# Kernel tuning notes

Measured on AMD Instinct MI355X. Metric: run time of the kernel, lower is better.

Reference implementation:

```python
import jax, jax.numpy as jnp
import numpy as np

B, T, I, H, L = 32768, 30, 4, 64, 32


def _lstm_layer(x, Wih, Whh, bih, bhh):
    """PyTorch-semantics single-layer LSTM, batch_first. Returns (outputs [B,T,H], h_T [B,H])."""
    # Precompute input contribution for all timesteps: [B, T, 4H]
    xg = jnp.einsum('bti,gi->btg', x, Wih) + bih + bhh
    Hh = Whh.shape[1]
    h0 = jnp.zeros((x.shape[0], Hh), x.dtype)

    def step(carry, xg_t):
        h, c = carry
        g = xg_t + h @ Whh.T  # [B, 4H]
        i, f, gg, o = jnp.split(g, 4, axis=-1)  # PyTorch gate order i,f,g,o
        c = jax.nn.sigmoid(f) * c + jax.nn.sigmoid(i) * jnp.tanh(gg)
        h = jax.nn.sigmoid(o) * jnp.tanh(c)
        return (h, c), h

    (hT, _), hs = jax.lax.scan(step, (h0, h0), jnp.swapaxes(xg, 0, 1))
    return jnp.swapaxes(hs, 0, 1), hT


def setup_inputs() -> dict:
    key = jax.random.key(0)
    ks = jax.random.split(key, 20)
    s = 0.1  # weight scale for numerical stability
    inp = {
        'x': jax.random.normal(ks[0], (B, T, I), jnp.float32),
        'enc1_Wih': s * jax.random.normal(ks[1], (4 * H, I), jnp.float32),
        'enc1_Whh': s * jax.random.normal(ks[2], (4 * H, H), jnp.float32),
        'enc1_bih': s * jax.random.normal(ks[3], (4 * H,), jnp.float32),
        'enc1_bhh': s * jax.random.normal(ks[4], (4 * H,), jnp.float32),
        'enc2_Wih': s * jax.random.normal(ks[5], (4 * L, H), jnp.float32),
        'enc2_Whh': s * jax.random.normal(ks[6], (4 * L, L), jnp.float32),
        'enc2_bih': s * jax.random.normal(ks[7], (4 * L,), jnp.float32),
        'enc2_bhh': s * jax.random.normal(ks[8], (4 * L,), jnp.float32),
        'dec1_Wih': s * jax.random.normal(ks[9], (4 * H, L), jnp.float32),
        'dec1_Whh': s * jax.random.normal(ks[10], (4 * H, H), jnp.float32),
        'dec1_bih': s * jax.random.normal(ks[11], (4 * H,), jnp.float32),
        'dec1_bhh': s * jax.random.normal(ks[12], (4 * H,), jnp.float32),
        'dec2_Wih': s * jax.random.normal(ks[13], (4 * I, H), jnp.float32),
        'dec2_Whh': s * jax.random.normal(ks[14], (4 * I, I), jnp.float32),
        'dec2_bih': s * jax.random.normal(ks[15], (4 * I,), jnp.float32),
        'dec2_bhh': s * jax.random.normal(ks[16], (4 * I,), jnp.float32),
    }
    return inp


def reference(x, enc1_Wih, enc1_Whh, enc1_bih, enc1_bhh,
              enc2_Wih, enc2_Whh, enc2_bih, enc2_bhh,
              dec1_Wih, dec1_Whh, dec1_bih, dec1_bhh,
              dec2_Wih, dec2_Whh, dec2_bih, dec2_bhh):
    seq_len = x.shape[1]
    out, _ = _lstm_layer(x, enc1_Wih, enc1_Whh, enc1_bih, enc1_bhh)
    out, h = _lstm_layer(out, enc2_Wih, enc2_Whh, enc2_bih, enc2_bhh)
    latent = jnp.repeat(h[:, None, :], seq_len, axis=1)  # [B, T, L]
    out, _ = _lstm_layer(latent, dec1_Wih, dec1_Whh, dec1_bih, dec1_bhh)
    out, _ = _lstm_layer(out, dec2_Wih, dec2_Whh, dec2_bih, dec2_bhh)
    return out
```

## Files before the change

kernel.cpp:

```cpp
#include <hip/hip_runtime.h>
#include <stdint.h>


typedef unsigned short u16;
typedef unsigned int u32;
typedef __attribute__((ext_vector_type(8))) short bf16x8;
typedef __attribute__((ext_vector_type(4))) float f32x4;
typedef __attribute__((ext_vector_type(4))) u32 u32x4;
typedef __attribute__((ext_vector_type(2))) u32 u32x2;

#define BATCH 32768
#define TT 30
#define IN 4
#define WAVES 8
#define BLOCKT (WAVES * 64)
#define MB 16
#define BPB (WAVES * MB)

#define LOG2E 1.4426950408889634f
#define LOG2E2 2.8853900817779268f

#define O_WHH1 0
#define O_W1C  8192
#define O_WIH2 9216
#define O_WHH2 13312
#define O_WHH3 0
#define O_WIH3 8192
#define O_WIH4 12288
#define O_W4HHF 12800
#define O_B1F 15360
#define O_B2F 15616
#define O_B3F 15744
#define O_B4F 16000
#define O_BUFS 16016
#define PBUF 1600
#define SMEM_WORDS (O_BUFS + WAVES * PBUF)
#define SMEM_BYTES (SMEM_WORDS * 4)

#define WB() __builtin_amdgcn_wave_barrier()
#define MFMA(a, b, c) __builtin_amdgcn_mfma_f32_16x16x32_bf16((a), (b), (c), 0, 0, 0)

__device__ __forceinline__ u16 f2bf(float f) {
    u32 u = __float_as_uint(f);
    u += 0x7fffu + ((u >> 16) & 1u);
    return (u16)(u >> 16);
}
__device__ __forceinline__ float bf2f(u16 v) { return __uint_as_float(((u32)v) << 16); }

__device__ __forceinline__ u32 cvtpk2(float a, float b) {
    u32 d;
    asm("v_cvt_pk_bf16_f32 %0, %1, %2" : "=v"(d) : "v"(a), "v"(b));
    return d;
}

__device__ __forceinline__ float unitH(float yi, float yf, float yg, float yo, float& c) {
    const float ei = __builtin_amdgcn_exp2f(-yi);
    const float ef = __builtin_amdgcn_exp2f(-yf);
    const float eg = __builtin_amdgcn_exp2f(yg);
    const float eo = __builtin_amdgcn_exp2f(-yo);
    const float Z = (1.f + ei) * (1.f + eg);
    const float X = 1.f + ef;
    const float num = fmaf(eg - 1.f, X, c * Z);
    c = num * __builtin_amdgcn_rcpf(X * Z);
    const float ec = __builtin_amdgcn_exp2f(c * LOG2E2);
    return (ec - 1.f) * __builtin_amdgcn_rcpf((1.f + eo) * (1.f + ec));
}

template <int KT, int GS>
__device__ __forceinline__ void stageBh(u16* hi, const float* src, int N, int tid) {
    const int K = KT * 32;
    const int total = N * K;
    for (int idx = tid; idx < total; idx += BLOCKT) {
        const int j = idx & 7;
        const int l = (idx >> 3) & 63;
        const int pr = idx >> 9;
        const int kt = pr & (KT - 1);
        const int nt = pr / KT;
        const int n = (nt << 4) | (l & 15);
        const int k = (kt << 5) + ((l >> 4) << 3) + j;
        const float s = (((n >> GS) & 3) == 2) ? LOG2E2 : LOG2E;
        hi[idx] = f2bf(src[n * K + k] * s);
    }
}

__global__ __launch_bounds__(BLOCKT)
__attribute__((amdgpu_waves_per_eu(2)))
void lstm_ae(
    const float* __restrict__ x,
    const float* __restrict__ w1ih, const float* __restrict__ w1hh,
    const float* __restrict__ b1i, const float* __restrict__ b1h,
    const float* __restrict__ w2ih, const float* __restrict__ w2hh,
    const float* __restrict__ b2i, const float* __restrict__ b2h,
    const float* __restrict__ w3ih, const float* __restrict__ w3hh,
    const float* __restrict__ b3i, const float* __restrict__ b3h,
    const float* __restrict__ w4ih, const float* __restrict__ w4hh,
    const float* __restrict__ b4i, const float* __restrict__ b4h,
    float* __restrict__ out) {
    extern __shared__ float smem[];
    float* W = smem;

    const int tid = threadIdx.x;
    const int wave = tid >> 6, lane = tid & 63;
    const int col = lane & 15, quad = lane >> 4;

    float* pb = smem + O_BUFS + wave * PBUF;
    u16* h1d = (u16*)pb;
    u16* h2b = (u16*)(pb + 1024);
    float* gbuf = pb + 1280;
    float* bufH4 = pb + 1536;

    const int b0w = blockIdx.x * BPB + wave * MB;
    const int hbase = (col << 3) + ((quad & 1) << 2) + ((quad >> 1) << 7);

    stageBh<2, 6>((u16*)(W + O_WHH1), w1hh, 256, tid);
    stageBh<2, 5>((u16*)(W + O_WIH2), w2ih, 128, tid);
    stageBh<1, 5>((u16*)(W + O_WHH2), w2hh, 128, tid);
    {
        u16* C = (u16*)(W + O_W1C);
        for (int idx = tid; idx < 2048; idx += BLOCKT) {
            const int n = idx >> 3, j = idx & 7;
            const float sc = ((n >> 6) == 2) ? LOG2E2 : LOG2E;
            const float w = w1ih[n * 4 + (j & 3)] * sc;
            C[idx] = (j < 4) ? f2bf(w) : f2bf(w - bf2f(f2bf(w)));
        }
    }
    float* b1f = W + O_B1F;
    float* b2f = W + O_B2F;
    float* b3f = W + O_B3F;
    float* b4f = W + O_B4F;
    for (int i = tid; i < 256; i += BLOCKT)
        b1f[i] = (b1i[i] + b1h[i]) * (((i >> 6) == 2) ? LOG2E2 : LOG2E);
    for (int i = tid; i < 128; i += BLOCKT)
        b2f[i] = (b2i[i] + b2h[i]) * (((i >> 5) == 2) ? LOG2E2 : LOG2E);
    for (int i = tid; i < 256; i += BLOCKT)
        b3f[i] = (b3i[i] + b3h[i]) * (((i >> 6) == 2) ? LOG2E2 : LOG2E);
    for (int i = tid; i < 16; i += BLOCKT)
        b4f[i] = (b4i[i] + b4h[i]) * (((i >> 2) == 2) ? LOG2E2 : LOG2E);
    {
        u32* z = (u32*)pb;
        for (int i = lane; i < 256; i += 64) z[1024 + i] = 0u;
        bufH4[lane] = 0.f;
    }
    __syncthreads();

    const u16* Whh1hi = (const u16*)(W + O_WHH1);
    const u16* Wih2hi = (const u16*)(W + O_WIH2);
    const u16* Whh2hi = (const u16*)(W + O_WHH2);
    const u16* W1cL = (const u16*)(W + O_W1C) + (col << 3) + ((quad == 1) ? 4 : 0);

    f32x4 b2r[8];
#pragma unroll
    for (int nt = 0; nt < 8; ++nt)
        b2r[nt] = *reinterpret_cast<const f32x4*>(b2f + nt * 16 + (quad << 2));

    float c1[4][4];
    float c2[2][4];
#pragma unroll
    for (int q = 0; q < 4; ++q)
#pragma unroll
        for (int r = 0; r < 4; ++r) c1[q][r] = 0.f;
#pragma unroll
    for (int q = 0; q < 2; ++q)
#pragma unroll
        for (int r = 0; r < 4; ++r) c2[q][r] = 0.f;

    float4 xcur = *reinterpret_cast<const float4*>(x + ((size_t)(b0w + col) * TT + 0) * IN);

    auto enc1_step = [&](const bf16x8 ah0, const bf16x8 ah1, u16* hnext, int tnext) {
        const float4 xc = xcur;
        {
            const int tn = (tnext + 1 < TT) ? tnext + 1 : tnext;
            xcur = *reinterpret_cast<const float4*>(x + ((size_t)(b0w + col) * TT + tn) * IN);
        }
        const u32 hi01 = cvtpk2(xc.x, xc.y);
        const u32 hi23 = cvtpk2(xc.z, xc.w);
        const float r0 = xc.x - __uint_as_float(hi01 << 16);
        const float r1 = xc.y - __uint_as_float(hi01 & 0xffff0000u);
        const float r2 = xc.z - __uint_as_float(hi23 << 16);
        const float r3 = xc.w - __uint_as_float(hi23 & 0xffff0000u);
        const u32 lo01 = cvtpk2(r0, r1);
        const u32 lo23 = cvtpk2(r2, r3);
        u32x4 xv;
        xv.x = (quad <= 1) ? hi01 : 0u;
        xv.y = (quad <= 1) ? hi23 : 0u;
        xv.z = (quad == 0) ? lo01 : 0u;
        xv.w = (quad == 0) ? lo23 : 0u;
        const bf16x8 a1x = __builtin_bit_cast(bf16x8, xv);
#pragma unroll
        for (int q = 0; q < 4; ++q) {
            f32x4 acc[4];
#pragma unroll
            for (int i = 0; i < 4; ++i) {
                const int nt = i * 4 + q;
                const u32x2 wp = *reinterpret_cast<const u32x2*>(W1cL + nt * 128);
                u32x4 afu;
                afu.x = wp.x; afu.y = wp.y; afu.z = wp.x; afu.w = wp.y;
                const bf16x8 af = __builtin_bit_cast(bf16x8, afu);
                const bf16x8 bh0 = *reinterpret_cast<const bf16x8*>(Whh1hi + ((nt * 2 + 0) * 64 + lane) * 8);
                const bf16x8 bh1 = *reinterpret_cast<const bf16x8*>(Whh1hi + ((nt * 2 + 1) * 64 + lane) * 8);
                f32x4 a = *reinterpret_cast<const f32x4*>(b1f + nt * 16 + (quad << 2));
                a = MFMA(af, a1x, a);
                a = MFMA(bh0, ah0, a);
                a = MFMA(bh1, ah1, a);
                acc[i] = a;
            }
            const float h0 = unitH(acc[0][0], acc[1][0], acc[2][0], acc[3][0], c1[q][0]);
            const float h1 = unitH(acc[0][1], acc[1][1], acc[2][1], acc[3][1], c1[q][1]);
            const float h2 = unitH(acc[0][2], acc[1][2], acc[2][2], acc[3][2], c1[q][2]);
            const float h3 = unitH(acc[0][3], acc[1][3], acc[2][3], acc[3][3], c1[q][3]);
            u32x2 wv;
            wv.x = cvtpk2(h0, h1);
            wv.y = cvtpk2(h2, h3);
            *reinterpret_cast<u32x2*>(hnext + hbase + ((q >> 1) << 9) + ((q & 1) << 8)) = wv;
        }
    };

    {
        const bf16x8 z8 = {};
        enc1_step(z8, z8, h1d, 0);
    }
    for (int t = 0; t < TT - 1; ++t) {
        const u16* hcur = h1d + ((t & 1) << 10);
        const bf16x8 ah0 = *reinterpret_cast<const bf16x8*>(hcur + lane * 8);
        const bf16x8 ah1 = *reinterpret_cast<const bf16x8*>(hcur + (64 + lane) * 8);
        const bf16x8 a2h = *reinterpret_cast<const bf16x8*>(h2b + lane * 8);
        f32x4 acc2[8];
#pragma unroll
        for (int nt = 0; nt < 8; ++nt) {
            const bf16x8 bh0 = *reinterpret_cast<const bf16x8*>(Wih2hi + ((nt * 2 + 0) * 64 + lane) * 8);
            const bf16x8 bh1 = *reinterpret_cast<const bf16x8*>(Wih2hi + ((nt * 2 + 1) * 64 + lane) * 8);
            const bf16x8 ch = *reinterpret_cast<const bf16x8*>(Whh2hi + (nt * 64 + lane) * 8);
            f32x4 a = b2r[nt];
            a = MFMA(bh0, ah0, a);
            a = MFMA(bh1, ah1, a);
            a = MFMA(ch, a2h, a);
            acc2[nt] = a;
        }
        enc1_step(ah0, ah1, h1d + (((t + 1) & 1) << 10), t + 1);
#pragma unroll
        for (int q = 0; q < 2; ++q) {
            const float h0 = unitH(acc2[q][0], acc2[2 + q][0], acc2[4 + q][0], acc2[6 + q][0], c2[q][0]);
            const float h1 = unitH(acc2[q][1], acc2[2 + q][1], acc2[4 + q][1], acc2[6 + q][1], c2[q][1]);
            const float h2 = unitH(acc2[q][2], acc2[2 + q][2], acc2[4 + q][2], acc2[6 + q][2], c2[q][2]);
            const float h3 = unitH(acc2[q][3], acc2[2 + q][3], acc2[4 + q][3], acc2[6 + q][3], c2[q][3]);
            u32x2 wv;
            wv.x = cvtpk2(h0, h1);
            wv.y = cvtpk2(h2, h3);
            *reinterpret_cast<u32x2*>(h2b + hbase + (q << 8)) = wv;
        }
    }
    {
        const u16* hcur = h1d + (((TT - 1) & 1) << 10);
        const bf16x8 ah0 = *reinterpret_cast<const bf16x8*>(hcur + lane * 8);
        const bf16x8 ah1 = *reinterpret_cast<const bf16x8*>(hcur + (64 + lane) * 8);
        const bf16x8 a2h = *reinterpret_cast<const bf16x8*>(h2b + lane * 8);
        f32x4 acc2[8];
#pragma unroll
        for (int nt = 0; nt < 8; ++nt) {
            const bf16x8 bh0 = *reinterpret_cast<const bf16x8*>(Wih2hi + ((nt * 2 + 0) * 64 + lane) * 8);
            const bf16x8 bh1 = *reinterpret_cast<const bf16x8*>(Wih2hi + ((nt * 2 + 1) * 64 + lane) * 8);
            const bf16x8 ch = *reinterpret_cast<const bf16x8*>(Whh2hi + (nt * 64 + lane) * 8);
            f32x4 a = b2r[nt];
            a = MFMA(bh0, ah0, a);
            a = MFMA(bh1, ah1, a);
            a = MFMA(ch, a2h, a);
            acc2[nt] = a;
        }
#pragma unroll
        for (int q = 0; q < 2; ++q) {
            const float h0 = unitH(acc2[q][0], acc2[2 + q][0], acc2[4 + q][0], acc2[6 + q][0], c2[q][0]);
            const float h1 = unitH(acc2[q][1], acc2[2 + q][1], acc2[4 + q][1], acc2[6 + q][1], c2[q][1]);
            const float h2 = unitH(acc2[q][2], acc2[2 + q][2], acc2[4 + q][2], acc2[6 + q][2], c2[q][2]);
            const float h3 = unitH(acc2[q][3], acc2[2 + q][3], acc2[4 + q][3], acc2[6 + q][3], c2[q][3]);
            u32x2 wv;
            wv.x = cvtpk2(h0, h1);
            wv.y = cvtpk2(h2, h3);
            *reinterpret_cast<u32x2*>(h2b + hbase + (q << 8)) = wv;
        }
    }

    __syncthreads();
    stageBh<2, 6>((u16*)(W + O_WHH3), w3hh, 256, tid);
    stageBh<1, 6>((u16*)(W + O_WIH3), w3ih, 256, tid);
    stageBh<2, 2>((u16*)(W + O_WIH4), w4ih, 16, tid);
    for (int i = tid; i < 64; i += BLOCKT)
        W[O_W4HHF + i] = w4hh[i] * ((((i >> 4) & 3) == 2) ? LOG2E2 : LOG2E);

    const bf16x8 aLh = *reinterpret_cast<const bf16x8*>(h2b + lane * 8);
    float c3[4][4];
#pragma unroll
    for (int q = 0; q < 4; ++q)
#pragma unroll
        for (int r = 0; r < 4; ++r) c3[q][r] = 0.f;
    float c4 = 0.f;
    const int u4 = lane & 3, mb = lane >> 2;
    __syncthreads();

    const u16* Whh3hi = (const u16*)(W + O_WHH3);
    const u16* Wih3hi = (const u16*)(W + O_WIH3);
    f32x4 b3r[16];
#pragma unroll
    for (int nt = 0; nt < 16; ++nt)
        b3r[nt] = *reinterpret_cast<const f32x4*>(b3f + nt * 16 + (quad << 2));
    const f32x4 bias4v = *reinterpret_cast<const f32x4*>(b4f + (quad << 2));
    const bf16x8 w4f0 = *reinterpret_cast<const bf16x8*>((const u16*)(W + O_WIH4) + (0 * 64 + lane) * 8);
    const bf16x8 w4f1 = *reinterpret_cast<const bf16x8*>((const u16*)(W + O_WIH4) + (1 * 64 + lane) * 8);
    float4 w4r[4];
#pragma unroll
    for (int r = 0; r < 4; ++r)
        w4r[r] = *reinterpret_cast<const float4*>(W + O_W4HHF + ((quad * 4 + r) << 2));

    auto dec1_step = [&](const bf16x8 ah0, const bf16x8 ah1, u16* hnext) {
#pragma unroll
        for (int q = 0; q < 4; ++q) {
            f32x4 acc[4];
#pragma unroll
            for (int i = 0; i < 4; ++i) {
                const int nt = i * 4 + q;
                const bf16x8 bL = *reinterpret_cast<const bf16x8*>(Wih3hi + (nt * 64 + lane) * 8);
                const bf16x8 bh0 = *reinterpret_cast<const bf16x8*>(Whh3hi + ((nt * 2 + 0) * 64 + lane) * 8);
                const bf16x8 bh1 = *reinterpret_cast<const bf16x8*>(Whh3hi + ((nt * 2 + 1) * 64 + lane) * 8);
                f32x4 a = MFMA(bL, aLh, b3r[nt]);
                a = MFMA(bh0, ah0, a);
                a = MFMA(bh1, ah1, a);
                acc[i] = a;
            }
            const float h0 = unitH(acc[0][0], acc[1][0], acc[2][0], acc[3][0], c3[q][0]);
            const float h1 = unitH(acc[0][1], acc[1][1], acc[2][1], acc[3][1], c3[q][1]);
            const float h2 = unitH(acc[0][2], acc[1][2], acc[2][2], acc[3][2], c3[q][2]);
            const float h3 = unitH(acc[0][3], acc[1][3], acc[2][3], acc[3][3], c3[q][3]);
            u32x2 wv;
            wv.x = cvtpk2(h0, h1);
            wv.y = cvtpk2(h2, h3);
            *reinterpret_cast<u32x2*>(hnext + hbase + ((q >> 1) << 9) + ((q & 1) << 8)) = wv;
        }
    };

    {
        const bf16x8 z8 = {};
        dec1_step(z8, z8, h1d);
    }
    for (int t = 0; t < TT - 1; ++t) {
        const u16* hcur = h1d + ((t & 1) << 10);
        const bf16x8 ah0 = *reinterpret_cast<const bf16x8*>(hcur + lane * 8);
        const bf16x8 ah1 = *reinterpret_cast<const bf16x8*>(hcur + (64 + lane) * 8);
        f32x4 acc4 = bias4v;
        {
            const float4 hv = *reinterpret_cast<const float4*>(bufH4 + (col << 2));
#pragma unroll
            for (int r = 0; r < 4; ++r) {
                float sa = acc4[r];
                sa = fmaf(w4r[r].x, hv.x, sa);
                sa = fmaf(w4r[r].y, hv.y, sa);
                sa = fmaf(w4r[r].z, hv.z, sa);
                sa = fmaf(w4r[r].w, hv.w, sa);
                acc4[r] = sa;
            }
        }
        acc4 = MFMA(w4f0, ah0, acc4);
        acc4 = MFMA(w4f1, ah1, acc4);
        dec1_step(ah0, ah1, h1d + (((t + 1) & 1) << 10));
        WB();
        *reinterpret_cast<f32x4*>(gbuf + (col << 4) + (quad << 2)) = acc4;
        WB();
        {
            const float yi = gbuf[mb * 16 + u4];
            const float yf = gbuf[mb * 16 + 4 + u4];
            const float yg = gbuf[mb * 16 + 8 + u4];
            const float yo = gbuf[mb * 16 + 12 + u4];
            const float h = unitH(yi, yf, yg, yo, c4);
            out[((size_t)(b0w + mb) * TT + t) * IN + u4] = h;
            bufH4[mb * 4 + u4] = h;
        }
    }
    {
        const int t = TT - 1;
        const u16* hcur = h1d + ((t & 1) << 10);
        const bf16x8 ah0 = *reinterpret_cast<const bf16x8*>(hcur + lane * 8);
        const bf16x8 ah1 = *reinterpret_cast<const bf16x8*>(hcur + (64 + lane) * 8);
        f32x4 acc4 = bias4v;
        {
            const float4 hv = *reinterpret_cast<const float4*>(bufH4 + (col << 2));
#pragma unroll
            for (int r = 0; r < 4; ++r) {
                float sa = acc4[r];
                sa = fmaf(w4r[r].x, hv.x, sa);
                sa = fmaf(w4r[r].y, hv.y, sa);
                sa = fmaf(w4r[r].z, hv.z, sa);
                sa = fmaf(w4r[r].w, hv.w, sa);
                acc4[r] = sa;
            }
        }
        acc4 = MFMA(w4f0, ah0, acc4);
        acc4 = MFMA(w4f1, ah1, acc4);
        WB();
        *reinterpret_cast<f32x4*>(gbuf + (col << 4) + (quad << 2)) = acc4;
        WB();
        {
            const float yi = gbuf[mb * 16 + u4];
            const float yf = gbuf[mb * 16 + 4 + u4];
            const float yg = gbuf[mb * 16 + 8 + u4];
            const float yo = gbuf[mb * 16 + 12 + u4];
            const float h = unitH(yi, yf, yg, yo, c4);
            out[((size_t)(b0w + mb) * TT + t) * IN + u4] = h;
        }
    }
}

extern "C" void kernel_launch(void* const* d_in, const int* in_sizes, int n_in,
                              void* d_out, int out_size, void* d_ws, size_t ws_size,
                              hipStream_t stream) {
    (void)in_sizes; (void)n_in; (void)d_ws; (void)ws_size; (void)out_size;
    hipFuncSetAttribute(reinterpret_cast<const void*>(lstm_ae),
                        hipFuncAttributeMaxDynamicSharedMemorySize, SMEM_BYTES);
    const float* xi = (const float*)d_in[0];
    const float* w1ih = (const float*)d_in[1];
    const float* w1hh = (const float*)d_in[2];
    const float* b1i = (const float*)d_in[3];
    const float* b1h = (const float*)d_in[4];
    const float* w2ih = (const float*)d_in[5];
    const float* w2hh = (const float*)d_in[6];
    const float* b2i = (const float*)d_in[7];
    const float* b2h = (const float*)d_in[8];
    const float* w3ih = (const float*)d_in[9];
    const float* w3hh = (const float*)d_in[10];
    const float* b3i = (const float*)d_in[11];
    const float* b3h = (const float*)d_in[12];
    const float* w4ih = (const float*)d_in[13];
    const float* w4hh = (const float*)d_in[14];
    const float* b4i = (const float*)d_in[15];
    const float* b4h = (const float*)d_in[16];
    float* out = (float*)d_out;

    lstm_ae<<<dim3(BATCH / BPB), dim3(BLOCKT), SMEM_BYTES, stream>>>(
        xi, w1ih, w1hh, b1i, b1h, w2ih, w2hh, b2i, b2h,
        w3ih, w3hh, b3i, b3h, w4ih, w4hh, b4i, b4h, out);
}
```

Measured before the change: 299.2 us.

## Interleave LSTM gate MFMAs with activation tails and fold enc1 bias into MFMA

```diff
diff --git a/kernel.cpp b/kernel.cpp
--- a/kernel.cpp
+++ b/kernel.cpp
@@ -22,17 +22,16 @@
 
 #define O_WHH1 0
 #define O_W1C  8192
-#define O_WIH2 9216
-#define O_WHH2 13312
+#define O_WIH2 10240
+#define O_WHH2 14336
 #define O_WHH3 0
 #define O_WIH3 8192
 #define O_WIH4 12288
 #define O_W4HHF 12800
-#define O_B1F 15360
-#define O_B2F 15616
-#define O_B3F 15744
-#define O_B4F 16000
-#define O_BUFS 16016
+#define O_B2F 16384
+#define O_B3F 16512
+#define O_B4F 16768
+#define O_BUFS 16784
 #define PBUF 1600
 #define SMEM_WORDS (O_BUFS + WAVES * PBUF)
 #define SMEM_BYTES (SMEM_WORDS * 4)
@@ -82,6 +81,74 @@
         hi[idx] = f2bf(src[n * K + k] * s);
     }
 }
+
+#define ENC1_MFMA(Q, ACC, A1X, AH0, AH1)                                                   \
+    _Pragma("unroll") for (int i_ = 0; i_ < 4; ++i_) {                                     \
+        const int nt_ = i_ * 4 + (Q);                                                      \
+        const bf16x8 bh0_ = *reinterpret_cast<const bf16x8*>(Whh1hi + ((nt_ * 2 + 0) * 64 + lane) * 8); \
+        const bf16x8 bh1_ = *reinterpret_cast<const bf16x8*>(Whh1hi + ((nt_ * 2 + 1) * 64 + lane) * 8); \
+        f32x4 a_ = MFMA(w1a[nt_], (A1X), zf);                                              \
+        a_ = MFMA(bh0_, (AH0), a_);                                                        \
+        a_ = MFMA(bh1_, (AH1), a_);                                                        \
+        (ACC)[i_] = a_;                                                                    \
+    }
+
+#define ENC1_TAIL(Q, ACC, HOUT) {                                                          \
+        const float h0_ = unitH((ACC)[0][0], (ACC)[1][0], (ACC)[2][0], (ACC)[3][0], c1[Q][0]); \
+        const float h1_ = unitH((ACC)[0][1], (ACC)[1][1], (ACC)[2][1], (ACC)[3][1], c1[Q][1]); \
+        const float h2_ = unitH((ACC)[0][2], (ACC)[1][2], (ACC)[2][2], (ACC)[3][2], c1[Q][2]); \
+        const float h3_ = unitH((ACC)[0][3], (ACC)[1][3], (ACC)[2][3], (ACC)[3][3], c1[Q][3]); \
+        u32x2 wv_;                                                                         \
+        wv_.x = cvtpk2(h0_, h1_);                                                          \
+        wv_.y = cvtpk2(h2_, h3_);                                                          \
+        *reinterpret_cast<u32x2*>((HOUT) + hbase + (((Q) >> 1) << 9) + (((Q) & 1) << 8)) = wv_; \
+    }
+
+#define ENC2_BURST(AH0, AH1, A2H, ACC2)                                                    \
+    _Pragma("unroll") for (int nt_ = 0; nt_ < 8; ++nt_) {                                  \
+        const bf16x8 bh0_ = *reinterpret_cast<const bf16x8*>(Wih2hi + ((nt_ * 2 + 0) * 64 + lane) * 8); \
+        const bf16x8 bh1_ = *reinterpret_cast<const bf16x8*>(Wih2hi + ((nt_ * 2 + 1) * 64 + lane) * 8); \
+        const bf16x8 ch_ = *reinterpret_cast<const bf16x8*>(Whh2hi + (nt_ * 64 + lane) * 8); \
+        f32x4 a_ = b2r[nt_];                                                               \
+        a_ = MFMA(bh0_, (AH0), a_);                                                        \
+        a_ = MFMA(bh1_, (AH1), a_);                                                        \
+        a_ = MFMA(ch_, (A2H), a_);                                                         \
+        (ACC2)[nt_] = a_;                                                                  \
+    }
+
+#define ENC2_TAIL(ACC2)                                                                    \
+    _Pragma("unroll") for (int q_ = 0; q_ < 2; ++q_) {                                     \
+        const float h0_ = unitH((ACC2)[q_][0], (ACC2)[2 + q_][0], (ACC2)[4 + q_][0], (ACC2)[6 + q_][0], c2[q_][0]); \
+        const float h1_ = unitH((ACC2)[q_][1], (ACC2)[2 + q_][1], (ACC2)[4 + q_][1], (ACC2)[6 + q_][1], c2[q_][1]); \
+        const float h2_ = unitH((ACC2)[q_][2], (ACC2)[2 + q_][2], (ACC2)[4 + q_][2], (ACC2)[6 + q_][2], c2[q_][2]); \
+        const float h3_ = unitH((ACC2)[q_][3], (ACC2)[2 + q_][3], (ACC2)[4 + q_][3], (ACC2)[6 + q_][3], c2[q_][3]); \
+        u32x2 wv_;                                                                         \
+        wv_.x = cvtpk2(h0_, h1_);                                                          \
+        wv_.y = cvtpk2(h2_, h3_);                                                          \
+        *reinterpret_cast<u32x2*>(h2b + hbase + (q_ << 8)) = wv_;                          \
+    }
+
+#define DEC1_MFMA(Q, ACC, AH0, AH1)                                                        \
+    _Pragma("unroll") for (int i_ = 0; i_ < 4; ++i_) {                                     \
+        const int nt_ = i_ * 4 + (Q);                                                      \
+        const bf16x8 bh0_ = *reinterpret_cast<const bf16x8*>(Whh3hi + ((nt_ * 2 + 0) * 64 + lane) * 8); \
+        const bf16x8 bh1_ = *reinterpret_cast<const bf16x8*>(Whh3hi + ((nt_ * 2 + 1) * 64 + lane) * 8); \
+        f32x4 a_ = MFMA(wih3r[nt_], aLh, b3r[nt_]);                                        \
+        a_ = MFMA(bh0_, (AH0), a_);                                                        \
+        a_ = MFMA(bh1_, (AH1), a_);                                                        \
+        (ACC)[i_] = a_;                                                                    \
+    }
+
+#define DEC1_TAIL(Q, ACC, HOUT) {                                                          \
+        const float h0_ = unitH((ACC)[0][0], (ACC)[1][0], (ACC)[2][0], (ACC)[3][0], c3[Q][0]); \
+        const float h1_ = unitH((ACC)[0][1], (ACC)[1][1], (ACC)[2][1], (ACC)[3][1], c3[Q][1]); \
+        const float h2_ = unitH((ACC)[0][2], (ACC)[1][2], (ACC)[2][2], (ACC)[3][2], c3[Q][2]); \
+        const float h3_ = unitH((ACC)[0][3], (ACC)[1][3], (ACC)[2][3], (ACC)[3][3], c3[Q][3]); \
+        u32x2 wv_;                                                                         \
+        wv_.x = cvtpk2(h0_, h1_);                                                          \
+        wv_.y = cvtpk2(h2_, h3_);                                                          \
+        *reinterpret_cast<u32x2*>((HOUT) + hbase + (((Q) >> 1) << 9) + (((Q) & 1) << 8)) = wv_; \
+    }
 
 __global__ __launch_bounds__(BLOCKT)
 __attribute__((amdgpu_waves_per_eu(2)))
@@ -117,19 +184,27 @@
     stageBh<1, 5>((u16*)(W + O_WHH2), w2hh, 128, tid);
     {
         u16* C = (u16*)(W + O_W1C);
-        for (int idx = tid; idx < 2048; idx += BLOCKT) {
-            const int n = idx >> 3, j = idx & 7;
+        for (int idx = tid; idx < 256 * 16; idx += BLOCKT) {
+            const int n = idx >> 4, j = idx & 15;
             const float sc = ((n >> 6) == 2) ? LOG2E2 : LOG2E;
-            const float w = w1ih[n * 4 + (j & 3)] * sc;
-            C[idx] = (j < 4) ? f2bf(w) : f2bf(w - bf2f(f2bf(w)));
-        }
-    }
-    float* b1f = W + O_B1F;
+            u16 v = 0;
+            if (j < 4) {
+                v = f2bf(w1ih[n * 4 + j] * sc);
+            } else if (j < 8) {
+                const float w = w1ih[n * 4 + (j - 4)] * sc;
+                v = f2bf(w - bf2f(f2bf(w)));
+            } else if (j == 8) {
+                v = f2bf((b1i[n] + b1h[n]) * sc);
+            } else if (j == 9) {
+                const float b = (b1i[n] + b1h[n]) * sc;
+                v = f2bf(b - bf2f(f2bf(b)));
+            }
+            C[idx] = v;
+        }
+    }
     float* b2f = W + O_B2F;
     float* b3f = W + O_B3F;
     float* b4f = W + O_B4F;
-    for (int i = tid; i < 256; i += BLOCKT)
-        b1f[i] = (b1i[i] + b1h[i]) * (((i >> 6) == 2) ? LOG2E2 : LOG2E);
     for (int i = tid; i < 128; i += BLOCKT)
         b2f[i] = (b2i[i] + b2h[i]) * (((i >> 5) == 2) ? LOG2E2 : LOG2E);
     for (int i = tid; i < 256; i += BLOCKT)
@@ -146,8 +221,26 @@
     const u16* Whh1hi = (const u16*)(W + O_WHH1);
     const u16* Wih2hi = (const u16*)(W + O_WIH2);
     const u16* Whh2hi = (const u16*)(W + O_WHH2);
-    const u16* W1cL = (const u16*)(W + O_W1C) + (col << 3) + ((quad == 1) ? 4 : 0);
-
+
+    bf16x8 w1a[16];
+    {
+        const u16* Cx = (const u16*)(W + O_W1C);
+#pragma unroll
+        for (int nt = 0; nt < 16; ++nt) {
+            const u16* row = Cx + (((nt << 4) | col) << 4);
+            u32x4 v = {0u, 0u, 0u, 0u};
+            if (quad == 0) {
+                const u32x2 p = *reinterpret_cast<const u32x2*>(row);
+                v.x = p.x; v.y = p.y; v.z = p.x; v.w = p.y;
+            } else if (quad == 1) {
+                const u32x2 p = *reinterpret_cast<const u32x2*>(row + 4);
+                v.x = p.x; v.y = p.y; v.z = p.x; v.w = p.y;
+            } else if (quad == 2) {
+                v.x = *reinterpret_cast<const u32*>(row + 8);
+            }
+            w1a[nt] = __builtin_bit_cast(bf16x8, v);
+        }
+    }
     f32x4 b2r[8];
 #pragma unroll
     for (int nt = 0; nt < 8; ++nt)
@@ -164,14 +257,10 @@
 #pragma unroll
         for (int r = 0; r < 4; ++r) c2[q][r] = 0.f;
 
+    const f32x4 zf = {0.f, 0.f, 0.f, 0.f};
     float4 xcur = *reinterpret_cast<const float4*>(x + ((size_t)(b0w + col) * TT + 0) * IN);
 
-    auto enc1_step = [&](const bf16x8 ah0, const bf16x8 ah1, u16* hnext, int tnext) {
-        const float4 xc = xcur;
-        {
-            const int tn = (tnext + 1 < TT) ? tnext + 1 : tnext;
-            xcur = *reinterpret_cast<const float4*>(x + ((size_t)(b0w + col) * TT + tn) * IN);
-        }
+    auto buildX = [&](const float4 xc) -> bf16x8 {
         const u32 hi01 = cvtpk2(xc.x, xc.y);
         const u32 hi23 = cvtpk2(xc.z, xc.w);
         const float r0 = xc.x - __uint_as_float(hi01 << 16);
@@ -181,73 +270,51 @@
         const u32 lo01 = cvtpk2(r0, r1);
         const u32 lo23 = cvtpk2(r2, r3);
         u32x4 xv;
-        xv.x = (quad <= 1) ? hi01 : 0u;
+        xv.x = (quad <= 1) ? hi01 : ((quad == 2) ? 0x3F803F80u : 0u);
         xv.y = (quad <= 1) ? hi23 : 0u;
         xv.z = (quad == 0) ? lo01 : 0u;
         xv.w = (quad == 0) ? lo23 : 0u;
-        const bf16x8 a1x = __builtin_bit_cast(bf16x8, xv);
-#pragma unroll
-        for (int q = 0; q < 4; ++q) {
-            f32x4 acc[4];
-#pragma unroll
-            for (int i = 0; i < 4; ++i) {
-                const int nt = i * 4 + q;
-                const u32x2 wp = *reinterpret_cast<const u32x2*>(W1cL + nt * 128);
-                u32x4 afu;
-                afu.x = wp.x; afu.y = wp.y; afu.z = wp.x; afu.w = wp.y;
-                const bf16x8 af = __builtin_bit_cast(bf16x8, afu);
-                const bf16x8 bh0 = *reinterpret_cast<const bf16x8*>(Whh1hi + ((nt * 2 + 0) * 64 + lane) * 8);
-                const bf16x8 bh1 = *reinterpret_cast<const bf16x8*>(Whh1hi + ((nt * 2 + 1) * 64 + lane) * 8);
-                f32x4 a = *reinterpret_cast<const f32x4*>(b1f + nt * 16 + (quad << 2));
-                a = MFMA(af, a1x, a);
-                a = MFMA(bh0, ah0, a);
-                a = MFMA(bh1, ah1, a);
-                acc[i] = a;
-            }
-            const float h0 = unitH(acc[0][0], acc[1][0], acc[2][0], acc[3][0], c1[q][0]);
-            const float h1 = unitH(acc[0][1], acc[1][1], acc[2][1], acc[3][1], c1[q][1]);
-            const float h2 = unitH(acc[0][2], acc[1][2], acc[2][2], acc[3][2], c1[q][2]);
-            const float h3 = unitH(acc[0][3], acc[1][3], acc[2][3], acc[3][3], c1[q][3]);
-            u32x2 wv;
-            wv.x = cvtpk2(h0, h1);
-            wv.y = cvtpk2(h2, h3);
-            *reinterpret_cast<u32x2*>(hnext + hbase + ((q >> 1) << 9) + ((q & 1) << 8)) = wv;
-        }
+        return __builtin_bit_cast(bf16x8, xv);
     };
 
     {
         const bf16x8 z8 = {};
-        enc1_step(z8, z8, h1d, 0);
+        const bf16x8 a1x = buildX(xcur);
+        xcur = *reinterpret_cast<const float4*>(x + ((size_t)(b0w + col) * TT + 1) * IN);
+        f32x4 accA[4], accB[4];
+        ENC1_MFMA(0, accA, a1x, z8, z8)
+        ENC1_MFMA(1, accB, a1x, z8, z8)
+        ENC1_TAIL(0, accA, h1d)
+        ENC1_MFMA(2, accA, a1x, z8, z8)
+        ENC1_TAIL(1, accB, h1d)
+        ENC1_MFMA(3, accB, a1x, z8, z8)
+        ENC1_TAIL(2, accA, h1d)
+        ENC1_TAIL(3, accB, h1d)
     }
     for (int t = 0; t < TT - 1; ++t) {
         const u16* hcur = h1d + ((t & 1) << 10);
+        u16* hnext = h1d + (((t + 1) & 1) << 10);
         const bf16x8 ah0 = *reinterpret_cast<const bf16x8*>(hcur + lane * 8);
         const bf16x8 ah1 = *reinterpret_cast<const bf16x8*>(hcur + (64 + lane) * 8);
         const bf16x8 a2h = *reinterpret_cast<const bf16x8*>(h2b + lane * 8);
         f32x4 acc2[8];
-#pragma unroll
-        for (int nt = 0; nt < 8; ++nt) {
-            const bf16x8 bh0 = *reinterpret_cast<const bf16x8*>(Wih2hi + ((nt * 2 + 0) * 64 + lane) * 8);
-            const bf16x8 bh1 = *reinterpret_cast<const bf16x8*>(Wih2hi + ((nt * 2 + 1) * 64 + lane) * 8);
-            const bf16x8 ch = *reinterpret_cast<const bf16x8*>(Whh2hi + (nt * 64 + lane) * 8);
-            f32x4 a = b2r[nt];
-            a = MFMA(bh0, ah0, a);
-            a = MFMA(bh1, ah1, a);
-            a = MFMA(ch, a2h, a);
-            acc2[nt] = a;
-        }
-        enc1_step(ah0, ah1, h1d + (((t + 1) & 1) << 10), t + 1);
-#pragma unroll
-        for (int q = 0; q < 2; ++q) {
-            const float h0 = unitH(acc2[q][0], acc2[2 + q][0], acc2[4 + q][0], acc2[6 + q][0], c2[q][0]);
-            const float h1 = unitH(acc2[q][1], acc2[2 + q][1], acc2[4 + q][1], acc2[6 + q][1], c2[q][1]);
-            const float h2 = unitH(acc2[q][2], acc2[2 + q][2], acc2[4 + q][2], acc2[6 + q][2], c2[q][2]);
-            const float h3 = unitH(acc2[q][3], acc2[2 + q][3], acc2[4 + q][3], acc2[6 + q][3], c2[q][3]);
-            u32x2 wv;
-            wv.x = cvtpk2(h0, h1);
-            wv.y = cvtpk2(h2, h3);
-            *reinterpret_cast<u32x2*>(h2b + hbase + (q << 8)) = wv;
-        }
+        ENC2_BURST(ah0, ah1, a2h, acc2)
+        const bf16x8 a1x = buildX(xcur);
+        {
+            const int tn = (t + 2 < TT) ? t + 2 : TT - 1;
+            xcur = *reinterpret_cast<const float4*>(x + ((size_t)(b0w + col) * TT + tn) * IN);
+        }
+        f32x4 accA[4], accB[4];
+        ENC1_MFMA(0, accA, a1x, ah0, ah1)
+        WB();
+        ENC2_TAIL(acc2)
+        ENC1_MFMA(1, accB, a1x, ah0, ah1)
+        ENC1_TAIL(0, accA, hnext)
+        ENC1_MFMA(2, accA, a1x, ah0, ah1)
+        ENC1_TAIL(1, accB, hnext)
+        ENC1_MFMA(3, accB, a1x, ah0, ah1)
+        ENC1_TAIL(2, accA, hnext)
+        ENC1_TAIL(3, accB, hnext)
     }
     {
         const u16* hcur = h1d + (((TT - 1) & 1) << 10);
@@ -255,28 +322,9 @@
         const bf16x8 ah1 = *reinterpret_cast<const bf16x8*>(hcur + (64 + lane) * 8);
         const bf16x8 a2h = *reinterpret_cast<const bf16x8*>(h2b + lane * 8);
         f32x4 acc2[8];
-#pragma unroll
-        for (int nt = 0; nt < 8; ++nt) {
-            const bf16x8 bh0 = *reinterpret_cast<const bf16x8*>(Wih2hi + ((nt * 2 + 0) * 64 + lane) * 8);
-            const bf16x8 bh1 = *reinterpret_cast<const bf16x8*>(Wih2hi + ((nt * 2 + 1) * 64 + lane) * 8);
-            const bf16x8 ch = *reinterpret_cast<const bf16x8*>(Whh2hi + (nt * 64 + lane) * 8);
-            f32x4 a = b2r[nt];
-            a = MFMA(bh0, ah0, a);
-            a = MFMA(bh1, ah1, a);
-            a = MFMA(ch, a2h, a);
-            acc2[nt] = a;
-        }
-#pragma unroll
-        for (int q = 0; q < 2; ++q) {
-            const float h0 = unitH(acc2[q][0], acc2[2 + q][0], acc2[4 + q][0], acc2[6 + q][0], c2[q][0]);
-            const float h1 = unitH(acc2[q][1], acc2[2 + q][1], acc2[4 + q][1], acc2[6 + q][1], c2[q][1]);
-            const float h2 = unitH(acc2[q][2], acc2[2 + q][2], acc2[4 + q][2], acc2[6 + q][2], c2[q][2]);
-            const float h3 = unitH(acc2[q][3], acc2[2 + q][3], acc2[4 + q][3], acc2[6 + q][3], c2[q][3]);
-            u32x2 wv;
-            wv.x = cvtpk2(h0, h1);
-            wv.y = cvtpk2(h2, h3);
-            *reinterpret_cast<u32x2*>(h2b + hbase + (q << 8)) = wv;
-        }
+        ENC2_BURST(ah0, ah1, a2h, acc2)
+        WB();
+        ENC2_TAIL(acc2)
     }
 
     __syncthreads();
@@ -298,6 +346,10 @@
 
     const u16* Whh3hi = (const u16*)(W + O_WHH3);
     const u16* Wih3hi = (const u16*)(W + O_WIH3);
+    bf16x8 wih3r[16];
+#pragma unroll
+    for (int nt = 0; nt < 16; ++nt)
+        wih3r[nt] = *reinterpret_cast<const bf16x8*>(Wih3hi + (nt * 64 + lane) * 8);
     f32x4 b3r[16];
 #pragma unroll
     for (int nt = 0; nt < 16; ++nt)
@@ -310,38 +362,21 @@
     for (int r = 0; r < 4; ++r)
         w4r[r] = *reinterpret_cast<const float4*>(W + O_W4HHF + ((quad * 4 + r) << 2));
 
-    auto dec1_step = [&](const bf16x8 ah0, const bf16x8 ah1, u16* hnext) {
-#pragma unroll
-        for (int q = 0; q < 4; ++q) {
-            f32x4 acc[4];
-#pragma unroll
-            for (int i = 0; i < 4; ++i) {
-                const int nt = i * 4 + q;
-                const bf16x8 bL = *reinterpret_cast<const bf16x8*>(Wih3hi + (nt * 64 + lane) * 8);
-                const bf16x8 bh0 = *reinterpret_cast<const bf16x8*>(Whh3hi + ((nt * 2 + 0) * 64 + lane) * 8);
-                const bf16x8 bh1 = *reinterpret_cast<const bf16x8*>(Whh3hi + ((nt * 2 + 1) * 64 + lane) * 8);
-                f32x4 a = MFMA(bL, aLh, b3r[nt]);
-                a = MFMA(bh0, ah0, a);
-                a = MFMA(bh1, ah1, a);
-                acc[i] = a;
-            }
-            const float h0 = unitH(acc[0][0], acc[1][0], acc[2][0], acc[3][0], c3[q][0]);
-            const float h1 = unitH(acc[0][1], acc[1][1], acc[2][1], acc[3][1], c3[q][1]);
-            const float h2 = unitH(acc[0][2], acc[1][2], acc[2][2], acc[3][2], c3[q][2]);
-            const float h3 = unitH(acc[0][3], acc[1][3], acc[2][3], acc[3][3], c3[q][3]);
-            u32x2 wv;
-            wv.x = cvtpk2(h0, h1);
-            wv.y = cvtpk2(h2, h3);
-            *reinterpret_cast<u32x2*>(hnext + hbase + ((q >> 1) << 9) + ((q & 1) << 8)) = wv;
-        }
-    };
-
     {
         const bf16x8 z8 = {};
-        dec1_step(z8, z8, h1d);
+        f32x4 accA[4], accB[4];
+        DEC1_MFMA(0, accA, z8, z8)
+        DEC1_MFMA(1, accB, z8, z8)
+        DEC1_TAIL(0, accA, h1d)
+        DEC1_MFMA(2, accA, z8, z8)
+        DEC1_TAIL(1, accB, h1d)
+        DEC1_MFMA(3, accB, z8, z8)
+        DEC1_TAIL(2, accA, h1d)
+        DEC1_TAIL(3, accB, h1d)
     }
     for (int t = 0; t < TT - 1; ++t) {
         const u16* hcur = h1d + ((t & 1) << 10);
+        u16* hnext = h1d + (((t + 1) & 1) << 10);
         const bf16x8 ah0 = *reinterpret_cast<const bf16x8*>(hcur + lane * 8);
         const bf16x8 ah1 = *reinterpret_cast<const bf16x8*>(hcur + (64 + lane) * 8);
         f32x4 acc4 = bias4v;
@@ -359,7 +394,8 @@
         }
         acc4 = MFMA(w4f0, ah0, acc4);
         acc4 = MFMA(w4f1, ah1, acc4);
-        dec1_step(ah0, ah1, h1d + (((t + 1) & 1) << 10));
+        f32x4 accA[4], accB[4];
+        DEC1_MFMA(0, accA, ah0, ah1)
         WB();
         *reinterpret_cast<f32x4*>(gbuf + (col << 4) + (quad << 2)) = acc4;
         WB();
@@ -372,6 +408,13 @@
             out[((size_t)(b0w + mb) * TT + t) * IN + u4] = h;
             bufH4[mb * 4 + u4] = h;
         }
+        DEC1_MFMA(1, accB, ah0, ah1)
+        DEC1_TAIL(0, accA, hnext)
+        DEC1_MFMA(2, accA, ah0, ah1)
+        DEC1_TAIL(1, accB, hnext)
+        DEC1_MFMA(3, accB, ah0, ah1)
+        DEC1_TAIL(2, accA, hnext)
+        DEC1_TAIL(3, accB, hnext)
     }
     {
         const int t = TT - 1;
```

Result: no change. 296.4 us (-0.9%).
